# Kernel optimization log

Measured on AMD Instinct MI355X. Metric: run time of the kernel, lower is better.

## Reference

```python
import jax, jax.numpy as jnp
import numpy as np
import math

DIM = 128
HEAD = 4
RANK = 32
HEAD_DIM = DIM // HEAD
B, T, N, F = 2, 128, 1024, 128  # t == f == dim required by the original module
EXPAND = 4
EPS = 1e-6


def setup_inputs() -> dict:
    key = jax.random.key(0)
    ks = jax.random.split(key, 12)
    s = 0.02
    return {
        "x": jax.random.normal(ks[0], (B, T, N, F), jnp.float32),
        "norm_w": jnp.ones((DIM,), jnp.float32),
        "q_w": jax.random.normal(ks[1], (DIM, DIM), jnp.float32) * s,   # (out,in)
        "q_b": jnp.zeros((DIM,), jnp.float32),
        "key_p": jax.random.normal(ks[2], (RANK, HEAD, HEAD_DIM), jnp.float32),
        "v_w": jax.random.normal(ks[3], (DIM, DIM), jnp.float32) * s,
        "v_b": jnp.zeros((DIM,), jnp.float32),
        "alpha": jnp.full((HEAD, 1), math.log(9.0), jnp.float32),
        "beta": jnp.full((HEAD, 1), math.log(0.01), jnp.float32),
        "w1": jax.random.normal(ks[4], (EXPAND * DIM, DIM), jnp.float32) * s,
        "b1": jnp.zeros((EXPAND * DIM,), jnp.float32),
        "w2": jax.random.normal(ks[5], (EXPAND * DIM, DIM), jnp.float32) * s,
        "b2": jnp.zeros((EXPAND * DIM,), jnp.float32),
        "w3": jax.random.normal(ks[6], (DIM, EXPAND * DIM), jnp.float32) * s,
        "b3": jnp.zeros((DIM,), jnp.float32),
    }


def _rmsnorm(x, w):
    # NOTE: original reduces over axis 1 (the t axis), weight broadcasts on last axis
    var = jnp.mean(x * x, axis=1, keepdims=True)
    return w * (x * jax.lax.rsqrt(var + EPS))


def _attention(x, q_w, q_b, key_p, v_w, v_b, alpha, beta):
    b, t, n, f = x.shape
    q = (jnp.einsum('btnf,of->btno', x, q_w) + q_b).reshape(b, t, n, HEAD, HEAD_DIM)
    attn = jnp.einsum('btnhd,rhd->btnhr', q, key_p) / (HEAD_DIM ** 0.5)
    xv = (jnp.einsum('btnf,of->btno', x, v_w) + v_b).reshape(b, t, n, HEAD, HEAD_DIM)
    # softmax over rank, aggregate values into landmarks
    v = jnp.einsum('btnhr,btnhd->btrhd', jax.nn.softmax(attn, axis=-1), xv)
    # softmax over node axis (axis=-3 of btnhr), scatter landmarks back to nodes
    v = jnp.einsum('btnhr,btrhd->btnhd', jax.nn.softmax(attn, axis=-3), v)
    v = jax.nn.sigmoid(alpha) * xv + jax.nn.sigmoid(beta) * v
    return v.reshape(b, t, n, f)


def _conv1x1(x, w, b):
    # Conv2d kernel_size=1 on (B, C=t, H=n, W=f)
    return jnp.einsum('oc,bcnf->bonf', w, x) + b[None, :, None, None]


def _ffn(x, w1, b1, w2, b2, w3, b3):
    h = jax.nn.silu(_conv1x1(x, w1, b1)) * _conv1x1(x, w2, b2)
    return _conv1x1(h, w3, b3)  # dropout is identity in eval mode


def reference(x, norm_w, q_w, q_b, key_p, v_w, v_b, alpha, beta,
              w1, b1, w2, b2, w3, b3):
    x = _attention(_rmsnorm(x, norm_w), q_w, q_b, key_p, v_w, v_b, alpha, beta) + x
    x = _ffn(_rmsnorm(x, norm_w), w1, b1, w2, b2, w3, b3) + x
    return x
```

## Files before the change

kernel.cpp:

```cpp
#include <hip/hip_runtime.h>

#define DEV static __device__ __forceinline__

constexpr int Bc = 2, Tc = 128, Nc = 1024, Fc = 128, Hc = 4, Rc = 32, Dc = 32;
constexpr int NF  = Nc * Fc;
constexpr int TOK = Bc * Tc * Nc;
constexpr float EPSc = 1e-6f;
constexpr float RSD  = 0.17677669529663687f;

typedef __bf16 bf16x8 __attribute__((ext_vector_type(8)));
typedef float  f32x16 __attribute__((ext_vector_type(16)));
typedef unsigned short us8 __attribute__((ext_vector_type(8)));
typedef unsigned short us4 __attribute__((ext_vector_type(4)));

DEV unsigned short f2bu(float f) {
    unsigned u = __builtin_bit_cast(unsigned, f);
    u += 0x7fffu + ((u >> 16) & 1u);
    return (unsigned short)(u >> 16);
}
DEV float bu2f(unsigned short s) {
    return __builtin_bit_cast(float, ((unsigned)s) << 16);
}
DEV float sigmoidf_(float z) { return 1.f / (1.f + __expf(-z)); }
DEV f32x16 zero16() { f32x16 z;
#pragma unroll
    for (int i = 0; i < 16; i++) z[i] = 0.f;
    return z; }

__global__ void k_rms_f32(const float* __restrict__ x, float* __restrict__ inv) {
    int j = blockIdx.x * 256 + threadIdx.x;
    int b = j >> 17;
    int p = j & (NF - 1);
    const float* px = x + (size_t)b * Tc * NF + p;
    float s = 0.f;
#pragma unroll 8
    for (int t = 0; t < Tc; ++t) { float v = px[(size_t)t * NF]; s = fmaf(v, v, s); }
    inv[j] = rsqrtf(s * (1.f / Tc) + EPSc);
}

__global__ void k_cvt(const float* __restrict__ w, unsigned short* __restrict__ o, int n) {
    int i = blockIdx.x * 256 + threadIdx.x;
    if (i < n) o[i] = f2bu(w[i]);
}
__global__ void k_cvt3(const float* __restrict__ w1, const float* __restrict__ w2,
                       const float* __restrict__ w3, unsigned short* __restrict__ o) {
    int i = blockIdx.x * 256 + threadIdx.x;
    float v;
    if (i < 65536)       v = w1[i];
    else if (i < 131072) v = w2[i - 65536];
    else                 v = w3[i - 131072];
    o[i] = f2bu(v);
}

__global__ void k_qk(const float* __restrict__ q_w, const float* __restrict__ q_b,
                     const float* __restrict__ key_p, const float* __restrict__ v_b,
                     unsigned short* __restrict__ Wcat, float* __restrict__ bias)
{
    __shared__ float sqw[32][128];
    __shared__ float skp[32][32];
    int h = blockIdx.x, tid = threadIdx.x;
    for (int i = tid; i < 4096; i += 256) {
        int d = i >> 7, c = i & 127;
        sqw[d][c] = q_w[(size_t)(h * 32 + d) * 128 + c];
    }
    for (int i = tid; i < 1024; i += 256) {
        int r = i >> 5, d = i & 31;
        skp[r][d] = key_p[(size_t)(r * 4 + h) * 32 + d] * RSD;
    }
    __syncthreads();
    int r = tid >> 3;
    int c0 = (tid & 7) * 16;
    for (int cc = 0; cc < 16; ++cc) {
        int c = c0 + cc;
        float s = 0.f;
#pragma unroll
        for (int d = 0; d < 32; ++d) s = fmaf(sqw[d][c], skp[r][d], s);
        Wcat[(size_t)(h * 32 + r) * 128 + c] = f2bu(s);
    }
    if (tid < 32) {
        float s = 0.f;
#pragma unroll
        for (int d = 0; d < 32; ++d) s = fmaf(q_b[h * 32 + d], skp[tid][d], s);
        bias[h * 32 + tid] = s;
    }
    if (h == 0 && tid >= 64 && tid < 192) bias[128 + tid - 64] = v_b[tid - 64];
}

__global__ __launch_bounds__(256, 4) void k_projm(
    const float* __restrict__ x, const float* __restrict__ inv1, const float* __restrict__ nw,
    const unsigned short* __restrict__ Wcat, const float* __restrict__ bias,
    unsigned short* __restrict__ Lb, unsigned short* __restrict__ XVb)
{
    const int tid = threadIdx.x, lane = tid & 63, wv = tid >> 6;
    const int lr = lane & 31, lhi = lane >> 5;
    const int tokb = blockIdx.x * 128 + wv * 32;
    const int tok = tokb + lr;
    const int b = tok >> 17, n = tok & 1023;
    const float* px = x + (size_t)tok * 128;
    const float* pi = inv1 + (size_t)b * NF + n * 128;

    bf16x8 af[8];
#pragma unroll
    for (int s = 0; s < 8; ++s) {
        const int c0 = s * 16 + lhi * 8;
        float4 xa = *(const float4*)(px + c0);
        float4 xb = *(const float4*)(px + c0 + 4);
        float4 ia = *(const float4*)(pi + c0);
        float4 ib = *(const float4*)(pi + c0 + 4);
        float4 na = *(const float4*)(nw + c0);
        float4 nb = *(const float4*)(nw + c0 + 4);
        bf16x8 v;
        v[0] = (__bf16)(xa.x * ia.x * na.x);
        v[1] = (__bf16)(xa.y * ia.y * na.y);
        v[2] = (__bf16)(xa.z * ia.z * na.z);
        v[3] = (__bf16)(xa.w * ia.w * na.w);
        v[4] = (__bf16)(xb.x * ib.x * nb.x);
        v[5] = (__bf16)(xb.y * ib.y * nb.y);
        v[6] = (__bf16)(xb.z * ib.z * nb.z);
        v[7] = (__bf16)(xb.w * ib.w * nb.w);
        af[s] = v;
    }

#pragma unroll
    for (int ot = 0; ot < 8; ++ot) {
        const unsigned short* pw = Wcat + (size_t)(ot * 32 + lr) * 128 + lhi * 8;
        f32x16 acc = zero16();
#pragma unroll
        for (int s = 0; s < 8; ++s) {
            bf16x8 bw = *(const bf16x8*)(pw + s * 16);
            acc = __builtin_amdgcn_mfma_f32_32x32x16_bf16(af[s], bw, acc, 0, 0, 0);
        }
        const int o = ot * 32 + lr;
        const float bv = bias[o];
        unsigned short* dst = (ot < 4) ? Lb : XVb;
        const int oo = (ot < 4) ? o : o - 128;
#pragma unroll
        for (int r = 0; r < 16; ++r) {
            const int trow = tokb + (r & 3) + 8 * (r >> 2) + 4 * lhi;
            dst[(size_t)trow * 128 + oo] = f2bu(acc[r] + bv);
        }
    }
}

__global__ __launch_bounds__(256, 4) void k_land(
    const unsigned short* __restrict__ Lb, const unsigned short* __restrict__ XVb,
    float* __restrict__ VL, float* __restrict__ M2, float* __restrict__ S2)
{
    __shared__ float sL [64][33];
    __shared__ float sXV[64][36];
    __shared__ float redm[32][8];
    __shared__ float reds[32][8];
    int tid = threadIdx.x;
    int blk = blockIdx.x;
    int h = blk & 3; int bt = blk >> 2;
    size_t base = (size_t)bt * Nc * 128 + h * 32;
    const int r_st = tid & 31, stripe = tid >> 5;
    const int ti = tid >> 2, sub = tid & 3;
    const int r_acc = tid >> 3, d0 = (tid & 7) * 4;
    float m_st = -1e30f, s_st = 0.f;
    float a0 = 0, a1 = 0, a2 = 0, a3 = 0;
    for (int n0 = 0; n0 < Nc; n0 += 64) {
        for (int k = tid; k < 2048; k += 256) {
            int i = k >> 5, rr = k & 31;
            size_t g = base + (size_t)(n0 + i) * 128 + rr;
            sL [i][rr] = bu2f(Lb [g]);
            sXV[i][rr] = bu2f(XVb[g]);
        }
        __syncthreads();
#pragma unroll
        for (int i8 = 0; i8 < 8; ++i8) {
            float v = sL[stripe * 8 + i8][r_st];
            float mn = fmaxf(m_st, v);
            s_st = s_st * __expf(m_st - mn) + __expf(v - mn);
            m_st = mn;
        }
        float e[8];
        float mx = -1e30f;
#pragma unroll
        for (int j = 0; j < 8; ++j) mx = fmaxf(mx, sL[ti][sub * 8 + j]);
        mx = fmaxf(mx, __shfl_xor(mx, 1));
        mx = fmaxf(mx, __shfl_xor(mx, 2));
        float sm = 0.f;
#pragma unroll
        for (int j = 0; j < 8; ++j) { e[j] = __expf(sL[ti][sub * 8 + j] - mx); sm += e[j]; }
        sm += __shfl_xor(sm, 1);
        sm += __shfl_xor(sm, 2);
        float iv = 1.f / sm;
        __syncthreads();
#pragma unroll
        for (int j = 0; j < 8; ++j) sL[ti][sub * 8 + j] = e[j] * iv;
        __syncthreads();
#pragma unroll 2
        for (int i = 0; i < 64; ++i) {
            float p = sL[i][r_acc];
            float4 v = *(const float4*)&sXV[i][d0];
            a0 = fmaf(p, v.x, a0); a1 = fmaf(p, v.y, a1);
            a2 = fmaf(p, v.z, a2); a3 = fmaf(p, v.w, a3);
        }
        __syncthreads();
    }
    redm[r_st][stripe] = m_st;
    reds[r_st][stripe] = s_st;
    __syncthreads();
    if (tid < 32) {
        float m = -1e30f;
#pragma unroll
        for (int k = 0; k < 8; ++k) m = fmaxf(m, redm[tid][k]);
        float s = 0.f;
#pragma unroll
        for (int k = 0; k < 8; ++k) s += reds[tid][k] * __expf(redm[tid][k] - m);
        M2[blk * 32 + tid] = m;
        S2[blk * 32 + tid] = s;
    }
    *(float4*)&VL[((size_t)blk * 32 + r_acc) * 32 + d0] = make_float4(a0, a1, a2, a3);
}

__global__ void k_out1(const float* __restrict__ x,
                       const unsigned short* __restrict__ Lb, const unsigned short* __restrict__ XVb,
                       const float* __restrict__ VL, const float* __restrict__ M2, const float* __restrict__ S2,
                       const float* __restrict__ alpha, const float* __restrict__ beta,
                       unsigned short* __restrict__ X2b)
{
    __shared__ float sVL[128][32];
    __shared__ float sP[8][128];
    __shared__ float sM[128], sSi[128], sAB[8];
    int tid = threadIdx.x;
    int tk0 = blockIdx.x * 8;
    int bt = tk0 >> 10;
    for (int k = tid; k < 4096; k += 256) sVL[k >> 5][k & 31] = VL[(size_t)bt * 4096 + k];
    if (tid < 128) { sM[tid] = M2[bt * 128 + tid]; sSi[tid] = 1.f / S2[bt * 128 + tid]; }
    if (tid < 8)   sAB[tid] = (tid < 4) ? sigmoidf_(alpha[tid]) : sigmoidf_(beta[tid - 4]);
    __syncthreads();
    for (int k = tid; k < 1024; k += 256) {
        int ti = k >> 7, f = k & 127;
        float lv = bu2f(Lb[(size_t)(tk0 + ti) * 128 + f]);
        sP[ti][f] = __expf(lv - sM[f]) * sSi[f];
    }
    __syncthreads();
    int ti = tid >> 5, quad = tid & 31;
    int h = quad >> 3, d0 = (quad & 7) * 4;
    float a0 = 0, a1 = 0, a2 = 0, a3 = 0;
    int hr0 = h * 32;
#pragma unroll 4
    for (int r = 0; r < 32; ++r) {
        float p = sP[ti][hr0 + r];
        float4 v = *(const float4*)&sVL[hr0 + r][d0];
        a0 = fmaf(p, v.x, a0); a1 = fmaf(p, v.y, a1);
        a2 = fmaf(p, v.z, a2); a3 = fmaf(p, v.w, a3);
    }
    size_t gi = (size_t)(tk0 + ti) * 128 + quad * 4;
    ushort4 xv4 = *(const ushort4*)&XVb[gi];
    float sa = sAB[h], sb = sAB[4 + h];
    float o0 = fmaf(sb, a0, fmaf(sa, bu2f(xv4.x), x[gi + 0]));
    float o1 = fmaf(sb, a1, fmaf(sa, bu2f(xv4.y), x[gi + 1]));
    float o2 = fmaf(sb, a2, fmaf(sa, bu2f(xv4.z), x[gi + 2]));
    float o3 = fmaf(sb, a3, fmaf(sa, bu2f(xv4.w), x[gi + 3]));
    ushort4 pk; pk.x = f2bu(o0); pk.y = f2bu(o1); pk.z = f2bu(o2); pk.w = f2bu(o3);
    *(ushort4*)&X2b[gi] = pk;
}

constexpr int XST = 132;
__global__ __launch_bounds__(256, 2) void k_ffn_mfma(
    const unsigned short* __restrict__ X2b, const float* __restrict__ nw,
    const unsigned short* __restrict__ w1b, const float* __restrict__ b1,
    const unsigned short* __restrict__ w2b, const float* __restrict__ b2,
    const unsigned short* __restrict__ w3b, const float* __restrict__ b3,
    float* __restrict__ out)
{
    __shared__ unsigned short smem[18432] __attribute__((aligned(16)));
    unsigned short* xstage = smem;
    unsigned short* gT     = smem;
    __shared__ float sscale[128];

    const int tid  = threadIdx.x;
    const int lane = tid & 63;
    const int wv   = tid >> 6;
    const int lr   = lane & 31;
    const int lhi  = lane >> 5;
    const int blk  = blockIdx.x;
    const int b    = blk >> 10, n = blk & 1023;

    const int mrow = (wv & 1) * 32;
    const int fh   = (wv >> 1) * 64;
    const int t0   = wv * 32;

    const unsigned short* xg = X2b + ((size_t)(b * Tc) * Nc + n) * 128;
#pragma unroll
    for (int p = 0; p < 8; ++p) {
        int i = p * 256 + tid;
        int t = i >> 4, fg = i & 15;
        us8 v = *(const us8*)(xg + (size_t)t * NF + fg * 8);
        int tt = t ^ ((fg & 7) << 3);
#pragma unroll
        for (int j = 0; j < 8; ++j) xstage[(fg * 8 + j) * XST + tt] = v[j];
    }
    __syncthreads();

    {
        int f = tid >> 1, half = tid & 1;
        int swz = ((f >> 3) & 7) << 3;
        float ss = 0.f;
#pragma unroll
        for (int kk = 0; kk < 8; ++kk) {
            int tb = (half * 64 + kk * 8) ^ swz;
            us4 u0 = *(const us4*)&xstage[f * XST + tb];
            us4 u1 = *(const us4*)&xstage[f * XST + tb + 4];
#pragma unroll
            for (int j = 0; j < 4; ++j) {
                float v0 = bu2f(u0[j]); ss = fmaf(v0, v0, ss);
                float v1 = bu2f(u1[j]); ss = fmaf(v1, v1, ss);
            }
        }
        ss += __shfl_xor(ss, 1);
        if (half == 0) sscale[f] = rsqrtf(ss * (1.f / Tc) + EPSc) * nw[f];
    }
    __syncthreads();

    bf16x8 xnf[2][8];
#pragma unroll
    for (int ft = 0; ft < 2; ++ft) {
        const int f = fh + ft * 32 + lr;
        const int swz = ((f >> 3) & 7) << 3;
        const float scale = sscale[f];
#pragma unroll
        for (int s = 0; s < 8; ++s) {
            int tb = (s * 16 + lhi * 8) ^ swz;
            us4 u0 = *(const us4*)&xstage[f * XST + tb];
            us4 u1 = *(const us4*)&xstage[f * XST + tb + 4];
            bf16x8 v;
#pragma unroll
            for (int j = 0; j < 4; ++j) {
                v[j]     = (__bf16)(bu2f(u0[j]) * scale);
                v[j + 4] = (__bf16)(bu2f(u1[j]) * scale);
            }
            xnf[ft][s] = v;
        }
    }
    __syncthreads();

    f32x16 oacc[4];
#pragma unroll
    for (int c = 0; c < 4; ++c) oacc[c] = zero16();

    const unsigned short* w1r = w1b + (size_t)(mrow + lr) * 128 + lhi * 8;
    const unsigned short* w2r = w2b + (size_t)(mrow + lr) * 128 + lhi * 8;
    const unsigned short* w3r = w3b + (size_t)(t0 + lr) * 512 + lhi * 8;

    int d = 0;
    for (int oc = 0; oc < 512; oc += 64) {
        bf16x8 a3[4];
        const unsigned short* pw3 = w3r + oc;
#pragma unroll
        for (int s = 0; s < 4; ++s) a3[s] = *(const bf16x8*)(pw3 + s * 16);

        f32x16 h1a = zero16(), h1b = zero16(), h2a = zero16(), h2b = zero16();
        const unsigned short* pw1 = w1r + (size_t)oc * 128;
        const unsigned short* pw2 = w2r + (size_t)oc * 128;
#pragma unroll
        for (int s = 0; s < 8; ++s) {
            bf16x8 a1 = *(const bf16x8*)(pw1 + s * 16);
            bf16x8 a2 = *(const bf16x8*)(pw2 + s * 16);
            h1a = __builtin_amdgcn_mfma_f32_32x32x16_bf16(a1, xnf[0][s], h1a, 0, 0, 0);
            h1b = __builtin_amdgcn_mfma_f32_32x32x16_bf16(a1, xnf[1][s], h1b, 0, 0, 0);
            h2a = __builtin_amdgcn_mfma_f32_32x32x16_bf16(a2, xnf[0][s], h2a, 0, 0, 0);
            h2b = __builtin_amdgcn_mfma_f32_32x32x16_bf16(a2, xnf[1][s], h2b, 0, 0, 0);
        }
        unsigned short* gTd = gT + d * 9216;
#pragma unroll
        for (int ft = 0; ft < 2; ++ft) {
            const int fcol = fh + ft * 32 + lr;
#pragma unroll
            for (int q = 0; q < 4; ++q) {
                ushort4 pk;
#pragma unroll
                for (int e = 0; e < 4; ++e) {
                    const int r = q * 4 + e;
                    const int orow = oc + mrow + e + 8 * q + 4 * lhi;
                    float z   = (ft ? h1b[r] : h1a[r]) + b1[orow];
                    float h2v = (ft ? h2b[r] : h2a[r]) + b2[orow];
                    float g   = z * sigmoidf_(z) * h2v;
                    unsigned short gb = f2bu(g);
                    if (e == 0) pk.x = gb; else if (e == 1) pk.y = gb;
                    else if (e == 2) pk.z = gb; else pk.w = gb;
                }
                const int o_l = mrow + 8 * q + 4 * lhi;
                *(ushort4*)&gTd[fcol * 72 + o_l] = pk;
            }
        }
        __syncthreads();
#pragma unroll
        for (int s = 0; s < 4; ++s) {
#pragma unroll
            for (int c = 0; c < 4; ++c) {
                bf16x8 bg = *(const bf16x8*)&gTd[(c * 32 + lr) * 72 + s * 16 + lhi * 8];
                oacc[c] = __builtin_amdgcn_mfma_f32_32x32x16_bf16(a3[s], bg, oacc[c], 0, 0, 0);
            }
        }
        d ^= 1;
    }

#pragma unroll
    for (int r = 0; r < 16; ++r) {
        const int t = t0 + (r & 3) + 8 * (r >> 2) + 4 * lhi;
        const float bt3 = b3[t];
        const size_t rowbase = ((size_t)(b * Tc + t) * Nc + n) * 128;
#pragma unroll
        for (int c = 0; c < 4; ++c) {
            const int f = c * 32 + lr;
            const size_t gi = rowbase + f;
            out[gi] = oacc[c][r] + bt3 + bu2f(X2b[gi]);
        }
    }
}

extern "C" void kernel_launch(void* const* d_in, const int* in_sizes, int n_in,
                              void* d_out, int out_size, void* d_ws, size_t ws_size,
                              hipStream_t stream) {
    const float* x      = (const float*)d_in[0];
    const float* norm_w = (const float*)d_in[1];
    const float* q_w    = (const float*)d_in[2];
    const float* q_b    = (const float*)d_in[3];
    const float* key_p  = (const float*)d_in[4];
    const float* v_w    = (const float*)d_in[5];
    const float* v_b    = (const float*)d_in[6];
    const float* alpha  = (const float*)d_in[7];
    const float* beta   = (const float*)d_in[8];
    const float* w1     = (const float*)d_in[9];
    const float* b1     = (const float*)d_in[10];
    const float* w2     = (const float*)d_in[11];
    const float* b2     = (const float*)d_in[12];
    const float* w3     = (const float*)d_in[13];
    const float* b3     = (const float*)d_in[14];
    float* out = (float*)d_out;

    char* ws = (char*)d_ws;
    float* inv1 = (float*)ws;
    float* inv2 = inv1 + (size_t)Bc * NF;
    float* VLp  = inv2 + (size_t)Bc * NF;
    float* M2p  = VLp + (size_t)Bc * Tc * Hc * Rc * Dc;
    float* S2p  = M2p + (size_t)Bc * Tc * Hc * Rc;
    unsigned short* Lb  = (unsigned short*)(S2p + (size_t)Bc * Tc * Hc * Rc);
    unsigned short* XVb = Lb  + (size_t)TOK * 128;
    unsigned short* X2b = XVb + (size_t)TOK * 128;

    unsigned short* Wcat = (unsigned short*)VLp;
    float* bias256 = VLp + 16384;

    unsigned short* w1bf = Lb;
    unsigned short* w2bf = Lb + 65536;
    unsigned short* w3bf = Lb + 131072;

    k_rms_f32 <<<Bc * NF / 256, 256, 0, stream>>>(x, inv1);
    k_qk      <<<4,             256, 0, stream>>>(q_w, q_b, key_p, v_b, Wcat, bias256);
    k_cvt     <<<64,            256, 0, stream>>>(v_w, Wcat + 16384, 16384);
    k_projm   <<<TOK / 128,     256, 0, stream>>>(x, inv1, norm_w, Wcat, bias256, Lb, XVb);
    k_land    <<<Bc * Tc * Hc,  256, 0, stream>>>(Lb, XVb, VLp, M2p, S2p);
    k_out1    <<<TOK / 8,       256, 0, stream>>>(x, Lb, XVb, VLp, M2p, S2p, alpha, beta, X2b);
    k_cvt3    <<<768,           256, 0, stream>>>(w1, w2, w3, w1bf);
    k_ffn_mfma<<<Bc * Nc,       256, 0, stream>>>(X2b, norm_w, w1bf, b1, w2bf, b2, w3bf, b3, out);
}
```

Baseline: 592.6 us.

## Vectorize loads, fuse weight conversion, and restructure FFN for higher occupancy

Folds the v_w bf16 conversion into the k_qk launch, vectorizes the bf16 tile loads in the landmark and output kernels, and restructures the FFN kernel. The FFN now computes one f-half at a time so fewer accumulators are live, raises launch bounds to 3 blocks, loads w3 fragments on demand, and seeds the output accumulator with the residual and bias taken from shared staging rather than global memory. The aim is to cut launch overhead, memory transactions and register pressure. The risk is spilling at the higher occupancy, or a wrong residual if the staged data differs from X2b.

```diff
diff --git a/kernel.cpp b/kernel.cpp
--- a/kernel.cpp
+++ b/kernel.cpp
@@ -38,10 +38,6 @@
     inv[j] = rsqrtf(s * (1.f / Tc) + EPSc);
 }
 
-__global__ void k_cvt(const float* __restrict__ w, unsigned short* __restrict__ o, int n) {
-    int i = blockIdx.x * 256 + threadIdx.x;
-    if (i < n) o[i] = f2bu(w[i]);
-}
 __global__ void k_cvt3(const float* __restrict__ w1, const float* __restrict__ w2,
                        const float* __restrict__ w3, unsigned short* __restrict__ o) {
     int i = blockIdx.x * 256 + threadIdx.x;
@@ -54,11 +50,18 @@
 
 __global__ void k_qk(const float* __restrict__ q_w, const float* __restrict__ q_b,
                      const float* __restrict__ key_p, const float* __restrict__ v_b,
+                     const float* __restrict__ v_w,
                      unsigned short* __restrict__ Wcat, float* __restrict__ bias)
 {
+    int blk = blockIdx.x, tid = threadIdx.x;
+    if (blk >= 4) {
+        int i = (blk - 4) * 256 + tid;
+        Wcat[16384 + i] = f2bu(v_w[i]);
+        return;
+    }
     __shared__ float sqw[32][128];
     __shared__ float skp[32][32];
-    int h = blockIdx.x, tid = threadIdx.x;
+    int h = blk;
     for (int i = tid; i < 4096; i += 256) {
         int d = i >> 7, c = i & 127;
         sqw[d][c] = q_w[(size_t)(h * 32 + d) * 128 + c];
@@ -146,7 +149,7 @@
     const unsigned short* __restrict__ Lb, const unsigned short* __restrict__ XVb,
     float* __restrict__ VL, float* __restrict__ M2, float* __restrict__ S2)
 {
-    __shared__ float sL [64][33];
+    __shared__ float sL [64][34];
     __shared__ float sXV[64][36];
     __shared__ float redm[32][8];
     __shared__ float reds[32][8];
@@ -154,17 +157,22 @@
     int blk = blockIdx.x;
     int h = blk & 3; int bt = blk >> 2;
     size_t base = (size_t)bt * Nc * 128 + h * 32;
+    const int li = tid >> 2, c8 = (tid & 3) * 8;
     const int r_st = tid & 31, stripe = tid >> 5;
     const int ti = tid >> 2, sub = tid & 3;
     const int r_acc = tid >> 3, d0 = (tid & 7) * 4;
     float m_st = -1e30f, s_st = 0.f;
     float a0 = 0, a1 = 0, a2 = 0, a3 = 0;
     for (int n0 = 0; n0 < Nc; n0 += 64) {
-        for (int k = tid; k < 2048; k += 256) {
-            int i = k >> 5, rr = k & 31;
-            size_t g = base + (size_t)(n0 + i) * 128 + rr;
-            sL [i][rr] = bu2f(Lb [g]);
-            sXV[i][rr] = bu2f(XVb[g]);
+        {
+            size_t g = base + (size_t)(n0 + li) * 128 + c8;
+            us8 vL = *(const us8*)(Lb + g);
+            us8 vX = *(const us8*)(XVb + g);
+#pragma unroll
+            for (int j = 0; j < 8; ++j) {
+                sL [li][c8 + j] = bu2f(vL[j]);
+                sXV[li][c8 + j] = bu2f(vX[j]);
+            }
         }
         __syncthreads();
 #pragma unroll
@@ -231,10 +239,12 @@
     if (tid < 128) { sM[tid] = M2[bt * 128 + tid]; sSi[tid] = 1.f / S2[bt * 128 + tid]; }
     if (tid < 8)   sAB[tid] = (tid < 4) ? sigmoidf_(alpha[tid]) : sigmoidf_(beta[tid - 4]);
     __syncthreads();
-    for (int k = tid; k < 1024; k += 256) {
-        int ti = k >> 7, f = k & 127;
-        float lv = bu2f(Lb[(size_t)(tk0 + ti) * 128 + f]);
-        sP[ti][f] = __expf(lv - sM[f]) * sSi[f];
+    {
+        int ti2 = tid >> 5, f4 = (tid & 31) * 4;
+        us4 lv = *(const us4*)&Lb[(size_t)(tk0 + ti2) * 128 + f4];
+#pragma unroll
+        for (int j = 0; j < 4; ++j)
+            sP[ti2][f4 + j] = __expf(bu2f(lv[j]) - sM[f4 + j]) * sSi[f4 + j];
     }
     __syncthreads();
     int ti = tid >> 5, quad = tid & 31;
@@ -260,7 +270,7 @@
 }
 
 constexpr int XST = 132;
-__global__ __launch_bounds__(256, 2) void k_ffn_mfma(
+__global__ __launch_bounds__(256, 3) void k_ffn_mfma(
     const unsigned short* __restrict__ X2b, const float* __restrict__ nw,
     const unsigned short* __restrict__ w1b, const float* __restrict__ b1,
     const unsigned short* __restrict__ w2b, const float* __restrict__ b2,
@@ -336,11 +346,22 @@
             xnf[ft][s] = v;
         }
     }
-    __syncthreads();
 
     f32x16 oacc[4];
 #pragma unroll
-    for (int c = 0; c < 4; ++c) oacc[c] = zero16();
+    for (int c = 0; c < 4; ++c) {
+        const int f = c * 32 + lr;
+        const int swz = ((f >> 3) & 7) << 3;
+#pragma unroll
+        for (int q = 0; q < 4; ++q) {
+            const int tb = t0 + 8 * q + 4 * lhi;
+            us4 u = *(const us4*)&xstage[f * XST + (tb ^ swz)];
+#pragma unroll
+            for (int e = 0; e < 4; ++e)
+                oacc[c][q * 4 + e] = bu2f(u[e]) + b3[tb + e];
+        }
+    }
+    __syncthreads();
 
     const unsigned short* w1r = w1b + (size_t)(mrow + lr) * 128 + lhi * 8;
     const unsigned short* w2r = w2b + (size_t)(mrow + lr) * 128 + lhi * 8;
@@ -348,26 +369,19 @@
 
     int d = 0;
     for (int oc = 0; oc < 512; oc += 64) {
-        bf16x8 a3[4];
-        const unsigned short* pw3 = w3r + oc;
-#pragma unroll
-        for (int s = 0; s < 4; ++s) a3[s] = *(const bf16x8*)(pw3 + s * 16);
-
-        f32x16 h1a = zero16(), h1b = zero16(), h2a = zero16(), h2b = zero16();
+        unsigned short* gTd = gT + d * 9216;
         const unsigned short* pw1 = w1r + (size_t)oc * 128;
         const unsigned short* pw2 = w2r + (size_t)oc * 128;
 #pragma unroll
-        for (int s = 0; s < 8; ++s) {
-            bf16x8 a1 = *(const bf16x8*)(pw1 + s * 16);
-            bf16x8 a2 = *(const bf16x8*)(pw2 + s * 16);
-            h1a = __builtin_amdgcn_mfma_f32_32x32x16_bf16(a1, xnf[0][s], h1a, 0, 0, 0);
-            h1b = __builtin_amdgcn_mfma_f32_32x32x16_bf16(a1, xnf[1][s], h1b, 0, 0, 0);
-            h2a = __builtin_amdgcn_mfma_f32_32x32x16_bf16(a2, xnf[0][s], h2a, 0, 0, 0);
-            h2b = __builtin_amdgcn_mfma_f32_32x32x16_bf16(a2, xnf[1][s], h2b, 0, 0, 0);
-        }
-        unsigned short* gTd = gT + d * 9216;
-#pragma unroll
         for (int ft = 0; ft < 2; ++ft) {
+            f32x16 h1 = zero16(), h2 = zero16();
+#pragma unroll
+            for (int s = 0; s < 8; ++s) {
+                bf16x8 a1 = *(const bf16x8*)(pw1 + s * 16);
+                bf16x8 a2 = *(const bf16x8*)(pw2 + s * 16);
+                h1 = __builtin_amdgcn_mfma_f32_32x32x16_bf16(a1, xnf[ft][s], h1, 0, 0, 0);
+                h2 = __builtin_amdgcn_mfma_f32_32x32x16_bf16(a2, xnf[ft][s], h2, 0, 0, 0);
+            }
             const int fcol = fh + ft * 32 + lr;
 #pragma unroll
             for (int q = 0; q < 4; ++q) {
@@ -376,8 +390,8 @@
                 for (int e = 0; e < 4; ++e) {
                     const int r = q * 4 + e;
                     const int orow = oc + mrow + e + 8 * q + 4 * lhi;
-                    float z   = (ft ? h1b[r] : h1a[r]) + b1[orow];
-                    float h2v = (ft ? h2b[r] : h2a[r]) + b2[orow];
+                    float z   = h1[r] + b1[orow];
+                    float h2v = h2[r] + b2[orow];
                     float g   = z * sigmoidf_(z) * h2v;
                     unsigned short gb = f2bu(g);
                     if (e == 0) pk.x = gb; else if (e == 1) pk.y = gb;
@@ -388,12 +402,14 @@
             }
         }
         __syncthreads();
+        const unsigned short* pw3 = w3r + oc;
 #pragma unroll
         for (int s = 0; s < 4; ++s) {
+            bf16x8 a3 = *(const bf16x8*)(pw3 + s * 16);
 #pragma unroll
             for (int c = 0; c < 4; ++c) {
                 bf16x8 bg = *(const bf16x8*)&gTd[(c * 32 + lr) * 72 + s * 16 + lhi * 8];
-                oacc[c] = __builtin_amdgcn_mfma_f32_32x32x16_bf16(a3[s], bg, oacc[c], 0, 0, 0);
+                oacc[c] = __builtin_amdgcn_mfma_f32_32x32x16_bf16(a3, bg, oacc[c], 0, 0, 0);
             }
         }
         d ^= 1;
@@ -402,13 +418,10 @@
 #pragma unroll
     for (int r = 0; r < 16; ++r) {
         const int t = t0 + (r & 3) + 8 * (r >> 2) + 4 * lhi;
-        const float bt3 = b3[t];
         const size_t rowbase = ((size_t)(b * Tc + t) * Nc + n) * 128;
 #pragma unroll
         for (int c = 0; c < 4; ++c) {
-            const int f = c * 32 + lr;
-            const size_t gi = rowbase + f;
-            out[gi] = oacc[c][r] + bt3 + bu2f(X2b[gi]);
+            out[rowbase + c * 32 + lr] = oacc[c][r];
         }
     }
 }
@@ -451,8 +464,7 @@
     unsigned short* w3bf = Lb + 131072;
 
     k_rms_f32 <<<Bc * NF / 256, 256, 0, stream>>>(x, inv1);
-    k_qk      <<<4,             256, 0, stream>>>(q_w, q_b, key_p, v_b, Wcat, bias256);
-    k_cvt     <<<64,            256, 0, stream>>>(v_w, Wcat + 16384, 16384);
+    k_qk      <<<68,            256, 0, stream>>>(q_w, q_b, key_p, v_b, v_w, Wcat, bias256);
     k_projm   <<<TOK / 128,     256, 0, stream>>>(x, inv1, norm_w, Wcat, bias256, Lb, XVb);
     k_land    <<<Bc * Tc * Hc,  256, 0, stream>>>(Lb, XVb, VLp, M2p, S2p);
     k_out1    <<<TOK / 8,       256, 0, stream>>>(x, Lb, XVb, VLp, M2p, S2p, alpha, beta, X2b);
```

New measurement: 801.4 us. 1.35x slower.
